# Optimization experiments

Measured on AMD Instinct MI355X. Metric: run time of the kernel, lower is better.

The kernel has to match this reference:

```python
import jax, jax.numpy as jnp
import numpy as np

N_NODES = 100000
N_EDGES = 640000
IN_CH, HID_CH, OUT_CH = 128, 256, 64


def setup_inputs() -> dict:
    key = jax.random.key(0)
    ks = jax.random.split(key, 6)
    x = jax.random.normal(ks[0], (N_NODES, IN_CH), dtype=jnp.float32)
    edge_index = jax.random.randint(ks[1], (2, N_EDGES), 0, N_NODES, dtype=jnp.int64)
    # Glorot-ish scaled weights
    W1l = jax.random.normal(ks[2], (HID_CH, IN_CH), dtype=jnp.float32) * (1.0 / np.sqrt(IN_CH))
    W1r = jax.random.normal(ks[3], (HID_CH, IN_CH), dtype=jnp.float32) * (1.0 / np.sqrt(IN_CH))
    W2l = jax.random.normal(ks[4], (OUT_CH, HID_CH), dtype=jnp.float32) * (1.0 / np.sqrt(HID_CH))
    W2r = jax.random.normal(ks[5], (OUT_CH, HID_CH), dtype=jnp.float32) * (1.0 / np.sqrt(HID_CH))
    b1 = jnp.zeros((HID_CH,), dtype=jnp.float32)
    b2 = jnp.zeros((OUT_CH,), dtype=jnp.float32)
    return {"x": x, "edge_index": edge_index, "W1l": W1l, "b1": b1, "W1r": W1r,
            "W2l": W2l, "b2": b2, "W2r": W2r}


def _sage_conv(x, src, dst, Wl, bl, Wr, n_nodes):
    # mean aggregation of source features at destination nodes (PyG aggr='mean')
    agg = jax.ops.segment_sum(x[src], dst, num_segments=n_nodes)          # [N, d]
    cnt = jax.ops.segment_sum(jnp.ones((src.shape[0], 1), x.dtype), dst,
                              num_segments=n_nodes)                        # [N, 1]
    mean = agg / jnp.maximum(cnt, 1.0)
    # out = lin_l(mean_neighbors) + lin_r(x); bias lives on lin_l
    return mean @ Wl.T + bl + x @ Wr.T


def reference(x, edge_index, W1l, b1, W1r, W2l, b2, W2r):
    src, dst = edge_index[0], edge_index[1]
    n = x.shape[0]
    h = _sage_conv(x, src, dst, W1l, b1, W1r, n)
    h = jax.nn.relu(h)
    out = _sage_conv(h, src, dst, W2l, b2, W2r, n)
    return out
```

## Files before the change

### kernel.cpp

```cpp
#include <hip/hip_runtime.h>


#define IN_CH  128
#define HID_CH 256
#define OUT_CH 64

typedef __bf16 bf16x8 __attribute__((ext_vector_type(8)));
typedef __bf16 bf16x4 __attribute__((ext_vector_type(4)));
typedef float  f32x4  __attribute__((ext_vector_type(4)));


__global__ void hist_kernel(const int* __restrict__ dst, int* __restrict__ deg, int E) {
    for (int e = blockIdx.x * blockDim.x + threadIdx.x; e < E; e += gridDim.x * blockDim.x)
        atomicAdd(&deg[dst[e]], 1);
}

__global__ void scan_block(const int* __restrict__ deg, int* __restrict__ offs,
                           int* __restrict__ bsum, int n) {
    __shared__ int s[512];
    int i = blockIdx.x * 512 + threadIdx.x;
    int v = (i < n) ? deg[i] : 0;
    s[threadIdx.x] = v;
    __syncthreads();
    #pragma unroll
    for (int d = 1; d < 512; d <<= 1) {
        int t = (threadIdx.x >= d) ? s[threadIdx.x - d] : 0;
        __syncthreads();
        s[threadIdx.x] += t;
        __syncthreads();
    }
    if (i < n) offs[i] = s[threadIdx.x] - v;
    if (threadIdx.x == 511) bsum[blockIdx.x] = s[511];
}

__global__ void scan_sums(int* __restrict__ bsum, int nb) {
    __shared__ int s[256];
    int v = (threadIdx.x < nb) ? bsum[threadIdx.x] : 0;
    s[threadIdx.x] = v;
    __syncthreads();
    #pragma unroll
    for (int d = 1; d < 256; d <<= 1) {
        int t = (threadIdx.x >= d) ? s[threadIdx.x - d] : 0;
        __syncthreads();
        s[threadIdx.x] += t;
        __syncthreads();
    }
    if (threadIdx.x < nb) bsum[threadIdx.x] = s[threadIdx.x] - v;
}

__global__ void scan_add(int* __restrict__ offs, const int* __restrict__ bsum, int n, int E) {
    int i = blockIdx.x * blockDim.x + threadIdx.x;
    if (i < n) offs[i] += bsum[i >> 9];
    if (i == 0) offs[n] = E;
}

__global__ void fill_csr(const int* __restrict__ src, const int* __restrict__ dst,
                         const int* __restrict__ offs, int* __restrict__ cur,
                         int* __restrict__ srcs, int E) {
    for (int e = blockIdx.x * blockDim.x + threadIdx.x; e < E; e += gridDim.x * blockDim.x) {
        int d = dst[e];
        int p = atomicAdd(&cur[d], 1);
        srcs[offs[d] + p] = src[e];
    }
}


__global__ void convert_weights(const float* __restrict__ W1l, const float* __restrict__ W1r,
                                const float* __restrict__ W2l, const float* __restrict__ W2r,
                                const float* __restrict__ b2,
                                __bf16* __restrict__ W1h, __bf16* __restrict__ W1lo,
                                __bf16* __restrict__ W2h, __bf16* __restrict__ W2lo,
                                float* __restrict__ bias2) {
    int i = blockIdx.x * 256 + threadIdx.x;
    if (i < 256 * 256) {
        int n = i >> 8, k = i & 255;
        float v = (k < 128) ? W1l[n * 128 + k] : W1r[n * 128 + (k - 128)];
        __bf16 h = (__bf16)v;
        W1h[i] = h; W1lo[i] = (__bf16)(v - (float)h);
    }
    if (i < 128 * 256) {
        int n = i >> 8, k = i & 255;
        float v = (n < 64) ? W2l[n * 256 + k] : W2r[(n - 64) * 256 + k];
        __bf16 h = (__bf16)v;
        W2h[i] = h; W2lo[i] = (__bf16)(v - (float)h);
    }
    if (i < 128) bias2[i] = (i < 64) ? 0.f : b2[i - 64];
}


__global__ __launch_bounds__(256) void agg_mean128(
    const float* __restrict__ X, const int* __restrict__ offs,
    const int* __restrict__ srcs, float* __restrict__ outm, int N) {
    int wv = (blockIdx.x * 256 + threadIdx.x) >> 6;
    int lane = threadIdx.x & 63;
    int grp = lane >> 5, l = lane & 31;
    int node = wv * 2 + grp;
    if (node >= N) return;
    int s0 = offs[node], s1 = offs[node + 1];
    float ax = 0.f, ay = 0.f, az = 0.f, aw = 0.f;
    int k = s0;
    for (; k + 4 <= s1; k += 4) {
        int i0 = srcs[k], i1 = srcs[k + 1], i2 = srcs[k + 2], i3 = srcs[k + 3];
        float4 a = *(const float4*)(X + (size_t)i0 * 128 + l * 4);
        float4 b = *(const float4*)(X + (size_t)i1 * 128 + l * 4);
        float4 c = *(const float4*)(X + (size_t)i2 * 128 + l * 4);
        float4 d = *(const float4*)(X + (size_t)i3 * 128 + l * 4);
        ax += (a.x + b.x) + (c.x + d.x);
        ay += (a.y + b.y) + (c.y + d.y);
        az += (a.z + b.z) + (c.z + d.z);
        aw += (a.w + b.w) + (c.w + d.w);
    }
    for (; k < s1; ++k) {
        int s = srcs[k];
        float4 a = *(const float4*)(X + (size_t)s * 128 + l * 4);
        ax += a.x; ay += a.y; az += a.z; aw += a.w;
    }
    int c = s1 - s0;
    float sc = 1.0f / (float)(c > 1 ? c : 1);
    float4 r; r.x = ax * sc; r.y = ay * sc; r.z = az * sc; r.w = aw * sc;
    *(float4*)(outm + (size_t)node * 128 + l * 4) = r;
}

__global__ __launch_bounds__(256) void agg_add_out(
    const float* __restrict__ Y2Z, const int* __restrict__ offs,
    const int* __restrict__ srcs, float* __restrict__ out, int N) {
    int wv = (blockIdx.x * 256 + threadIdx.x) >> 6;
    int lane = threadIdx.x & 63;
    int grp = lane >> 4, l = lane & 15;
    int node = wv * 4 + grp;
    if (node >= N) return;
    int s0 = offs[node], s1 = offs[node + 1];
    float4 z = *(const float4*)(Y2Z + (size_t)node * 128 + 64 + l * 4);
    float ax = 0.f, ay = 0.f, az = 0.f, aw = 0.f;
    int k = s0;
    for (; k + 4 <= s1; k += 4) {
        int i0 = srcs[k], i1 = srcs[k + 1], i2 = srcs[k + 2], i3 = srcs[k + 3];
        float4 a = *(const float4*)(Y2Z + (size_t)i0 * 128 + l * 4);
        float4 b = *(const float4*)(Y2Z + (size_t)i1 * 128 + l * 4);
        float4 c = *(const float4*)(Y2Z + (size_t)i2 * 128 + l * 4);
        float4 d = *(const float4*)(Y2Z + (size_t)i3 * 128 + l * 4);
        ax += (a.x + b.x) + (c.x + d.x);
        ay += (a.y + b.y) + (c.y + d.y);
        az += (a.z + b.z) + (c.z + d.z);
        aw += (a.w + b.w) + (c.w + d.w);
    }
    for (; k < s1; ++k) {
        int s = srcs[k];
        float4 a = *(const float4*)(Y2Z + (size_t)s * 128 + l * 4);
        ax += a.x; ay += a.y; az += a.z; aw += a.w;
    }
    int c = s1 - s0;
    float sc = 1.0f / (float)(c > 1 ? c : 1);
    float4 r;
    r.x = ax * sc + z.x; r.y = ay * sc + z.y;
    r.z = az * sc + z.z; r.w = aw * sc + z.w;
    *(float4*)(out + (size_t)node * 64 + l * 4) = r;
}


__global__ __launch_bounds__(256) void fused_l1l2(
    const float* __restrict__ mean1, const float* __restrict__ x,
    const __bf16* __restrict__ W1h, const __bf16* __restrict__ W1lo,
    const float* __restrict__ b1,
    const __bf16* __restrict__ W2h, const __bf16* __restrict__ W2lo,
    const float* __restrict__ bias2,
    float* __restrict__ Y2Z, int N) {
    __shared__ __align__(16) char lds[80 * 1024];
    __bf16* Hh    = (__bf16*)lds;
    __bf16* Hl    = (__bf16*)(lds + 32 * 1024);
    __bf16* W2hs  = (__bf16*)(lds + 64 * 1024);
    __bf16* W2ls  = (__bf16*)(lds + 72 * 1024);
    __bf16* Ah    = (__bf16*)lds;
    __bf16* Al    = (__bf16*)(lds + 4 * 1024);
    __bf16* B1h   = (__bf16*)(lds + 8 * 1024);
    __bf16* B1l   = (__bf16*)(lds + 24 * 1024);

    const int tid = threadIdx.x;
    const int lane = tid & 63;
    const int w = tid >> 6;
    const int l15 = lane & 15, lg = lane >> 4;
    const long row0 = (long)blockIdx.x * 64;

    f32x4 acc[4][4] = {};
    for (int k0 = 0; k0 < 256; k0 += 32) {
        const float* Asrc = (k0 < 128) ? mean1 : x;
        const int kk0 = (k0 < 128) ? k0 : k0 - 128;
        #pragma unroll
        for (int p = 0; p < 2; ++p) {
            int r = (tid >> 3) + p * 32;
            long gr = row0 + r;
            float4 v = make_float4(0.f, 0.f, 0.f, 0.f);
            if (gr < N) v = *(const float4*)(Asrc + gr * 128 + kk0 + (tid & 7) * 4);
            __bf16 h0 = (__bf16)v.x, h1 = (__bf16)v.y, h2 = (__bf16)v.z, h3 = (__bf16)v.w;
            bf16x4 hv, lv;
            hv[0] = h0; hv[1] = h1; hv[2] = h2; hv[3] = h3;
            lv[0] = (__bf16)(v.x - (float)h0); lv[1] = (__bf16)(v.y - (float)h1);
            lv[2] = (__bf16)(v.z - (float)h2); lv[3] = (__bf16)(v.w - (float)h3);
            int off = (r * 64 + (tid & 7) * 8) ^ (((r >> 1) & 3) << 4);
            *(bf16x4*)((char*)Ah + off) = hv;
            *(bf16x4*)((char*)Al + off) = lv;
        }
        #pragma unroll
        for (int p = 0; p < 4; ++p) {
            int n = (tid >> 2) + p * 64;
            long g = (long)n * 256 + k0 + (tid & 3) * 8;
            bf16x8 hv = *(const bf16x8*)(W1h + g);
            bf16x8 lv = *(const bf16x8*)(W1lo + g);
            int off = (n * 64 + (tid & 3) * 16) ^ (((n >> 1) & 3) << 4);
            *(bf16x8*)((char*)B1h + off) = hv;
            *(bf16x8*)((char*)B1l + off) = lv;
        }
        __syncthreads();
        bf16x8 ah[4], al[4], bh[4], bl[4];
        #pragma unroll
        for (int m = 0; m < 4; ++m) {
            int r = m * 16 + l15;
            int off = (r * 64 + lg * 16) ^ (((r >> 1) & 3) << 4);
            ah[m] = *(const bf16x8*)((char*)Ah + off);
            al[m] = *(const bf16x8*)((char*)Al + off);
        }
        #pragma unroll
        for (int n = 0; n < 4; ++n) {
            int rb = w * 64 + n * 16 + l15;
            int off = (rb * 64 + lg * 16) ^ (((rb >> 1) & 3) << 4);
            bh[n] = *(const bf16x8*)((char*)B1h + off);
            bl[n] = *(const bf16x8*)((char*)B1l + off);
        }
        #pragma unroll
        for (int m = 0; m < 4; ++m)
            #pragma unroll
            for (int n = 0; n < 4; ++n) {
                acc[m][n] = __builtin_amdgcn_mfma_f32_16x16x32_bf16(ah[m], bh[n], acc[m][n], 0, 0, 0);
                acc[m][n] = __builtin_amdgcn_mfma_f32_16x16x32_bf16(ah[m], bl[n], acc[m][n], 0, 0, 0);
                acc[m][n] = __builtin_amdgcn_mfma_f32_16x16x32_bf16(al[m], bh[n], acc[m][n], 0, 0, 0);
            }
        __syncthreads();
    }

    #pragma unroll
    for (int n = 0; n < 4; ++n) {
        int col = w * 64 + n * 16 + l15;
        float bv = b1[col];
        #pragma unroll
        for (int m = 0; m < 4; ++m) {
            #pragma unroll
            for (int rr = 0; rr < 4; ++rr) {
                int row = m * 16 + lg * 4 + rr;
                float v = fmaxf(acc[m][n][rr] + bv, 0.f);
                __bf16 hv = (__bf16)v;
                __bf16 lv = (__bf16)(v - (float)hv);
                int off = (row * 512 + col * 2) ^ ((row & 7) << 4);
                *(__bf16*)((char*)Hh + off) = hv;
                *(__bf16*)((char*)Hl + off) = lv;
            }
        }
    }
    __syncthreads();

    f32x4 acc2[4][2] = {};
    for (int k0 = 0; k0 < 256; k0 += 32) {
        #pragma unroll
        for (int p = 0; p < 2; ++p) {
            int n = (tid >> 2) + p * 64;
            long g = (long)n * 256 + k0 + (tid & 3) * 8;
            bf16x8 hv = *(const bf16x8*)(W2h + g);
            bf16x8 lv = *(const bf16x8*)(W2lo + g);
            int off = (n * 64 + (tid & 3) * 16) ^ (((n >> 1) & 3) << 4);
            *(bf16x8*)((char*)W2hs + off) = hv;
            *(bf16x8*)((char*)W2ls + off) = lv;
        }
        __syncthreads();
        bf16x8 a2h[4], a2l[4], b2h[2], b2l[2];
        #pragma unroll
        for (int m = 0; m < 4; ++m) {
            int row = m * 16 + l15;
            int off = (row * 512 + k0 * 2 + lg * 16) ^ ((row & 7) << 4);
            a2h[m] = *(const bf16x8*)((char*)Hh + off);
            a2l[m] = *(const bf16x8*)((char*)Hl + off);
        }
        #pragma unroll
        for (int n = 0; n < 2; ++n) {
            int rb = w * 32 + n * 16 + l15;
            int off = (rb * 64 + lg * 16) ^ (((rb >> 1) & 3) << 4);
            b2h[n] = *(const bf16x8*)((char*)W2hs + off);
            b2l[n] = *(const bf16x8*)((char*)W2ls + off);
        }
        #pragma unroll
        for (int m = 0; m < 4; ++m)
            #pragma unroll
            for (int n = 0; n < 2; ++n) {
                acc2[m][n] = __builtin_amdgcn_mfma_f32_16x16x32_bf16(a2h[m], b2h[n], acc2[m][n], 0, 0, 0);
                acc2[m][n] = __builtin_amdgcn_mfma_f32_16x16x32_bf16(a2h[m], b2l[n], acc2[m][n], 0, 0, 0);
                acc2[m][n] = __builtin_amdgcn_mfma_f32_16x16x32_bf16(a2l[m], b2h[n], acc2[m][n], 0, 0, 0);
            }
        __syncthreads();
    }

    #pragma unroll
    for (int n = 0; n < 2; ++n) {
        int gc = w * 32 + n * 16 + l15;
        float bv = bias2[gc];
        #pragma unroll
        for (int m = 0; m < 4; ++m) {
            #pragma unroll
            for (int rr = 0; rr < 4; ++rr) {
                long gr = row0 + m * 16 + lg * 4 + rr;
                if (gr < N) Y2Z[gr * 128 + gc] = acc2[m][n][rr] + bv;
            }
        }
    }
}


extern "C" void kernel_launch(void* const* d_in, const int* in_sizes, int n_in,
                              void* d_out, int out_size, void* d_ws, size_t ws_size,
                              hipStream_t stream) {
    const float* x   = (const float*)d_in[0];
    const int*   ei  = (const int*)d_in[1];
    const float* W1l = (const float*)d_in[2];
    const float* b1  = (const float*)d_in[3];
    const float* W1r = (const float*)d_in[4];
    const float* W2l = (const float*)d_in[5];
    const float* b2  = (const float*)d_in[6];
    const float* W2r = (const float*)d_in[7];
    float* out = (float*)d_out;

    const int N = in_sizes[0] / IN_CH;
    const int E = in_sizes[1] / 2;
    const int* src = ei;
    const int* dst = ei + E;

    float* buf1 = (float*)d_ws;
    float* buf2 = buf1 + (size_t)N * 128;
    int* deg  = (int*)(buf2 + (size_t)N * 128);
    int* offs = deg + N;
    int* cur  = offs + (N + 8);
    int* bsum = cur + N;
    int* srcs = bsum + 512;
    uintptr_t pp = (uintptr_t)(srcs + E);
    pp = (pp + 15) & ~(uintptr_t)15;
    __bf16* W1h  = (__bf16*)pp;
    __bf16* W1lo = W1h + 256 * 256;
    __bf16* W2h  = W1lo + 256 * 256;
    __bf16* W2lo = W2h + 128 * 256;
    float* bias2 = (float*)(W2lo + 128 * 256);

    hipMemsetAsync(deg, 0, sizeof(int) * N, stream);
    hipMemsetAsync(cur, 0, sizeof(int) * N, stream);

    convert_weights<<<256, 256, 0, stream>>>(W1l, W1r, W2l, W2r, b2,
                                             W1h, W1lo, W2h, W2lo, bias2);

    hist_kernel<<<1024, 256, 0, stream>>>(dst, deg, E);
    int nb = (N + 511) / 512;
    scan_block<<<nb, 512, 0, stream>>>(deg, offs, bsum, N);
    scan_sums<<<1, 256, 0, stream>>>(bsum, nb);
    scan_add<<<(N + 255) / 256, 256, 0, stream>>>(offs, bsum, N, E);
    fill_csr<<<1024, 256, 0, stream>>>(src, dst, offs, cur, srcs, E);

    agg_mean128<<<((N + 1) / 2 * 64 + 255) / 256, 256, 0, stream>>>(x, offs, srcs, buf1, N);

    fused_l1l2<<<(N + 63) / 64, 256, 0, stream>>>(buf1, x, W1h, W1lo, b1,
                                                  W2h, W2lo, bias2, buf2, N);

    agg_add_out<<<((N + 3) / 4 * 64 + 255) / 256, 256, 0, stream>>>(buf2, offs, srcs, out, N);
}
```

Before: 371.3 us.

## Load GEMM operands directly from global into registers, dropping LDS staging

The fused two-layer GEMM kernel now loads activation rows and weight fragments straight from global memory into MFMA operand registers instead of staging them through shared memory, and removes the per-k-step barriers. Only the hidden activation H stays in LDS, which cuts shared memory to 64KB, and launch bounds now request 2 blocks per CU. Each wave redundantly loads the same A rows (all 4 waves), and the weights go through cache. This trades LDS traffic and syncs for more global/L2 traffic and higher register pressure.

Measured after the change: 388.8 us. +4.7%, slower.

```diff
diff --git a/kernel.cpp b/kernel.cpp
--- a/kernel.cpp
+++ b/kernel.cpp
@@ -6,7 +6,6 @@
 #define OUT_CH 64
 
 typedef __bf16 bf16x8 __attribute__((ext_vector_type(8)));
-typedef __bf16 bf16x4 __attribute__((ext_vector_type(4)));
 typedef float  f32x4  __attribute__((ext_vector_type(4)));
 
 
@@ -158,22 +157,15 @@
 }
 
 
-__global__ __launch_bounds__(256) void fused_l1l2(
+__global__ __launch_bounds__(256, 2) void fused_l1l2(
     const float* __restrict__ mean1, const float* __restrict__ x,
     const __bf16* __restrict__ W1h, const __bf16* __restrict__ W1lo,
     const float* __restrict__ b1,
     const __bf16* __restrict__ W2h, const __bf16* __restrict__ W2lo,
     const float* __restrict__ bias2,
     float* __restrict__ Y2Z, int N) {
-    __shared__ __align__(16) char lds[80 * 1024];
-    __bf16* Hh    = (__bf16*)lds;
-    __bf16* Hl    = (__bf16*)(lds + 32 * 1024);
-    __bf16* W2hs  = (__bf16*)(lds + 64 * 1024);
-    __bf16* W2ls  = (__bf16*)(lds + 72 * 1024);
-    __bf16* Ah    = (__bf16*)lds;
-    __bf16* Al    = (__bf16*)(lds + 4 * 1024);
-    __bf16* B1h   = (__bf16*)(lds + 8 * 1024);
-    __bf16* B1l   = (__bf16*)(lds + 24 * 1024);
+    __shared__ __align__(16) __bf16 Hh[64 * 256];
+    __shared__ __align__(16) __bf16 Hl[64 * 256];
 
     const int tid = threadIdx.x;
     const int lane = tid & 63;
@@ -182,49 +174,40 @@
     const long row0 = (long)blockIdx.x * 64;
 
     f32x4 acc[4][4] = {};
-    for (int k0 = 0; k0 < 256; k0 += 32) {
-        const float* Asrc = (k0 < 128) ? mean1 : x;
-        const int kk0 = (k0 < 128) ? k0 : k0 - 128;
-        #pragma unroll
-        for (int p = 0; p < 2; ++p) {
-            int r = (tid >> 3) + p * 32;
-            long gr = row0 + r;
-            float4 v = make_float4(0.f, 0.f, 0.f, 0.f);
-            if (gr < N) v = *(const float4*)(Asrc + gr * 128 + kk0 + (tid & 7) * 4);
-            __bf16 h0 = (__bf16)v.x, h1 = (__bf16)v.y, h2 = (__bf16)v.z, h3 = (__bf16)v.w;
-            bf16x4 hv, lv;
-            hv[0] = h0; hv[1] = h1; hv[2] = h2; hv[3] = h3;
-            lv[0] = (__bf16)(v.x - (float)h0); lv[1] = (__bf16)(v.y - (float)h1);
-            lv[2] = (__bf16)(v.z - (float)h2); lv[3] = (__bf16)(v.w - (float)h3);
-            int off = (r * 64 + (tid & 7) * 8) ^ (((r >> 1) & 3) << 4);
-            *(bf16x4*)((char*)Ah + off) = hv;
-            *(bf16x4*)((char*)Al + off) = lv;
-        }
-        #pragma unroll
-        for (int p = 0; p < 4; ++p) {
-            int n = (tid >> 2) + p * 64;
-            long g = (long)n * 256 + k0 + (tid & 3) * 8;
-            bf16x8 hv = *(const bf16x8*)(W1h + g);
-            bf16x8 lv = *(const bf16x8*)(W1lo + g);
-            int off = (n * 64 + (tid & 3) * 16) ^ (((n >> 1) & 3) << 4);
-            *(bf16x8*)((char*)B1h + off) = hv;
-            *(bf16x8*)((char*)B1l + off) = lv;
-        }
-        __syncthreads();
-        bf16x8 ah[4], al[4], bh[4], bl[4];
+    #pragma unroll
+    for (int ks = 0; ks < 8; ++ks) {
+        const float* __restrict__ Asrc = (ks < 4) ? mean1 : x;
+        const int kk0 = ((ks < 4) ? ks * 32 : (ks - 4) * 32) + lg * 8;
+        const int k0 = ks * 32;
+
+        bf16x8 ah[4], al[4];
         #pragma unroll
         for (int m = 0; m < 4; ++m) {
-            int r = m * 16 + l15;
-            int off = (r * 64 + lg * 16) ^ (((r >> 1) & 3) << 4);
-            ah[m] = *(const bf16x8*)((char*)Ah + off);
-            al[m] = *(const bf16x8*)((char*)Al + off);
-        }
+            long gr = row0 + m * 16 + l15;
+            float4 v0 = make_float4(0.f, 0.f, 0.f, 0.f);
+            float4 v1 = make_float4(0.f, 0.f, 0.f, 0.f);
+            if (gr < N) {
+                v0 = *(const float4*)(Asrc + gr * 128 + kk0);
+                v1 = *(const float4*)(Asrc + gr * 128 + kk0 + 4);
+            }
+            float f0 = v0.x, f1 = v0.y, f2 = v0.z, f3 = v0.w;
+            float f4 = v1.x, f5 = v1.y, f6 = v1.z, f7 = v1.w;
+            bf16x8 h, l;
+            h[0] = (__bf16)f0; h[1] = (__bf16)f1; h[2] = (__bf16)f2; h[3] = (__bf16)f3;
+            h[4] = (__bf16)f4; h[5] = (__bf16)f5; h[6] = (__bf16)f6; h[7] = (__bf16)f7;
+            l[0] = (__bf16)(f0 - (float)h[0]); l[1] = (__bf16)(f1 - (float)h[1]);
+            l[2] = (__bf16)(f2 - (float)h[2]); l[3] = (__bf16)(f3 - (float)h[3]);
+            l[4] = (__bf16)(f4 - (float)h[4]); l[5] = (__bf16)(f5 - (float)h[5]);
+            l[6] = (__bf16)(f6 - (float)h[6]); l[7] = (__bf16)(f7 - (float)h[7]);
+            ah[m] = h; al[m] = l;
+        }
+        bf16x8 bh[4], bl[4];
         #pragma unroll
         for (int n = 0; n < 4; ++n) {
             int rb = w * 64 + n * 16 + l15;
-            int off = (rb * 64 + lg * 16) ^ (((rb >> 1) & 3) << 4);
-            bh[n] = *(const bf16x8*)((char*)B1h + off);
-            bl[n] = *(const bf16x8*)((char*)B1l + off);
+            long g = (long)rb * 256 + k0 + lg * 8;
+            bh[n] = *(const bf16x8*)(W1h + g);
+            bl[n] = *(const bf16x8*)(W1lo + g);
         }
         #pragma unroll
         for (int m = 0; m < 4; ++m)
@@ -234,7 +217,6 @@
                 acc[m][n] = __builtin_amdgcn_mfma_f32_16x16x32_bf16(ah[m], bl[n], acc[m][n], 0, 0, 0);
                 acc[m][n] = __builtin_amdgcn_mfma_f32_16x16x32_bf16(al[m], bh[n], acc[m][n], 0, 0, 0);
             }
-        __syncthreads();
     }
 
     #pragma unroll
@@ -258,19 +240,10 @@
     __syncthreads();
 
     f32x4 acc2[4][2] = {};
-    for (int k0 = 0; k0 < 256; k0 += 32) {
-        #pragma unroll
-        for (int p = 0; p < 2; ++p) {
-            int n = (tid >> 2) + p * 64;
-            long g = (long)n * 256 + k0 + (tid & 3) * 8;
-            bf16x8 hv = *(const bf16x8*)(W2h + g);
-            bf16x8 lv = *(const bf16x8*)(W2lo + g);
-            int off = (n * 64 + (tid & 3) * 16) ^ (((n >> 1) & 3) << 4);
-            *(bf16x8*)((char*)W2hs + off) = hv;
-            *(bf16x8*)((char*)W2ls + off) = lv;
-        }
-        __syncthreads();
-        bf16x8 a2h[4], a2l[4], b2h[2], b2l[2];
+    #pragma unroll
+    for (int ks = 0; ks < 8; ++ks) {
+        const int k0 = ks * 32;
+        bf16x8 a2h[4], a2l[4];
         #pragma unroll
         for (int m = 0; m < 4; ++m) {
             int row = m * 16 + l15;
@@ -278,22 +251,22 @@
             a2h[m] = *(const bf16x8*)((char*)Hh + off);
             a2l[m] = *(const bf16x8*)((char*)Hl + off);
         }
+        bf16x8 c2h[2], c2l[2];
         #pragma unroll
         for (int n = 0; n < 2; ++n) {
             int rb = w * 32 + n * 16 + l15;
-            int off = (rb * 64 + lg * 16) ^ (((rb >> 1) & 3) << 4);
-            b2h[n] = *(const bf16x8*)((char*)W2hs + off);
-            b2l[n] = *(const bf16x8*)((char*)W2ls + off);
+            long g = (long)rb * 256 + k0 + lg * 8;
+            c2h[n] = *(const bf16x8*)(W2h + g);
+            c2l[n] = *(const bf16x8*)(W2lo + g);
         }
         #pragma unroll
         for (int m = 0; m < 4; ++m)
             #pragma unroll
             for (int n = 0; n < 2; ++n) {
-                acc2[m][n] = __builtin_amdgcn_mfma_f32_16x16x32_bf16(a2h[m], b2h[n], acc2[m][n], 0, 0, 0);
-                acc2[m][n] = __builtin_amdgcn_mfma_f32_16x16x32_bf16(a2h[m], b2l[n], acc2[m][n], 0, 0, 0);
-                acc2[m][n] = __builtin_amdgcn_mfma_f32_16x16x32_bf16(a2l[m], b2h[n], acc2[m][n], 0, 0, 0);
-            }
-        __syncthreads();
+                acc2[m][n] = __builtin_amdgcn_mfma_f32_16x16x32_bf16(a2h[m], c2h[n], acc2[m][n], 0, 0, 0);
+                acc2[m][n] = __builtin_amdgcn_mfma_f32_16x16x32_bf16(a2h[m], c2l[n], acc2[m][n], 0, 0, 0);
+                acc2[m][n] = __builtin_amdgcn_mfma_f32_16x16x32_bf16(a2l[m], c2h[n], acc2[m][n], 0, 0, 0);
+            }
     }
 
     #pragma unroll
```
